# Kernel optimization log

Hardware: AMD Instinct MI355X
Metric: run time of the kernel (lower is better)

The kernel has to match this reference:

```python
import jax, jax.numpy as jnp
import numpy as np
from math import sqrt

DIM = 2048
N_HEADS = 2
HEAD_DIM = DIM // N_HEADS  # 1024 == RoPE dims (dim // 2)
ROPE_DIMS = DIM // 2
ROPE_BASE = 10000.0


def apply_rope(x, dims=ROPE_DIMS, base=ROPE_BASE, offset=0):
    # x: [B, H, L, Dh]; non-traditional (split-half) RoPE over sequence axis
    L = x.shape[-2]
    pos = jnp.arange(offset, offset + L, dtype=x.dtype)[:, None]          # [L,1]
    inv = jnp.exp(jnp.arange(0, dims, 2, dtype=x.dtype) * (-np.log(base) / dims))  # [dims//2]
    theta = pos * inv                                                      # [L, dims//2]
    cos, sin = jnp.cos(theta), jnp.sin(theta)
    h = dims // 2
    x1, x2 = x[..., :h], x[..., h:dims]
    rx1 = x1 * cos - x2 * sin
    rx2 = x1 * sin + x2 * cos
    if dims < x.shape[-1]:
        return jnp.concatenate([rx1, rx2, x[..., dims:]], axis=-1)
    return jnp.concatenate([rx1, rx2], axis=-1)


def setup_inputs() -> dict:
    key = jax.random.key(0)
    ks = jax.random.split(key, 6)
    B, L = 4, 2048
    x = jax.random.normal(ks[0], (B, L, DIM), dtype=jnp.float32)
    # causal additive mask
    causal = jnp.tril(jnp.ones((L, L), dtype=bool))
    mask = jnp.where(causal, 0.0, -1e9).astype(jnp.float32)
    s1 = 1.0 / sqrt(DIM)
    Wqkv_w = jax.random.normal(ks[1], (3 * DIM, DIM), dtype=jnp.float32) * s1
    Wqkv_b = jnp.zeros((3 * DIM,), dtype=jnp.float32)
    out_w = jax.random.normal(ks[2], (DIM, DIM), dtype=jnp.float32) * s1
    out_b = jnp.zeros((DIM,), dtype=jnp.float32)
    return {"x": x, "mask": mask, "Wqkv_w": Wqkv_w, "Wqkv_b": Wqkv_b,
            "out_w": out_w, "out_b": out_b}


def reference(x, mask, Wqkv_w, Wqkv_b, out_w, out_b):
    B, L, D = x.shape
    H, Dh = N_HEADS, HEAD_DIM
    qkv = x @ Wqkv_w.T + Wqkv_b                       # [B, L, 3D]
    q, k, v = jnp.split(qkv, 3, axis=-1)
    # b l (h d) -> b h l d
    split = lambda t: t.reshape(B, L, H, Dh).transpose(0, 2, 1, 3)
    q, k, v = split(q), split(k), split(v)
    q = apply_rope(q)
    k = apply_rope(k)
    scale = sqrt(1.0 / Dh)
    scores = jnp.einsum('bhld,bhkd->bhlk', q * scale, k)  # [B,H,L,L]
    scores = scores + mask                                 # additive causal mask
    probs = jax.nn.softmax(scores, axis=-1)
    vh = jnp.einsum('bhlk,bhkd->bhld', probs, v)
    vh = vh.transpose(0, 2, 1, 3).reshape(B, L, D)         # b h l d -> b l (h d)
    out = vh @ out_w.T + out_b
    return (out, k, v)
```

## Files before the change

kernel.cpp:

```cpp
#include <hip/hip_runtime.h>
#include <hip/hip_bf16.h>
#include <math.h>

typedef unsigned short u16;
typedef __attribute__((ext_vector_type(8))) __bf16 bf16x8;
typedef __attribute__((ext_vector_type(4))) float f32x4;

__device__ __forceinline__ u16 f2b(float f) {
  unsigned u = __builtin_bit_cast(unsigned, f);
  u += 0x7fffu + ((u >> 16) & 1u);
  return (u16)(u >> 16);
}
__device__ __forceinline__ float b2f(u16 h) {
  unsigned u = ((unsigned)h) << 16;
  return __builtin_bit_cast(float, u);
}

__device__ __forceinline__ void gld_lds16(const u16* g, u16* l) {
  __builtin_amdgcn_global_load_lds(
      (const __attribute__((address_space(1))) unsigned int*)g,
      (__attribute__((address_space(3))) unsigned int*)l, 16, 0, 0);
}

template <class FC>
__device__ __forceinline__ void gemm128_body(const u16* A, int lda,
                                             const u16* B, int ldb, FC fc,
                                             int m0, int n0, int K) {
  __shared__ __align__(16) u16 As[128 * 64];
  __shared__ __align__(16) u16 Bs[128 * 64];
  const int tid = threadIdx.x;
  const int wave = tid >> 6;
  const int lane = tid & 63;
  const int srow = lane >> 3;
  const int scol = ((lane & 7) ^ srow) * 8;
  const int wm = (wave & 1) * 64;
  const int wn = (wave >> 1) * 64;
  const int fm = lane & 15;
  const int fs = fm & 7;

  const u16* Abase = A + (size_t)m0 * lda;
  const u16* Bbase = B + (size_t)n0 * ldb;
  const size_t aLane = (size_t)(wave * 8 + srow) * lda + scol;
  const size_t bLane = (size_t)(wave * 8 + srow) * ldb + scol;

  f32x4 acc[4][4];
#pragma unroll
  for (int i = 0; i < 4; ++i)
#pragma unroll
    for (int j = 0; j < 4; ++j) acc[i][j] = (f32x4){0.f, 0.f, 0.f, 0.f};

  for (int k0 = 0; k0 < K; k0 += 64) {
#pragma unroll
    for (int c = 0; c < 4; ++c) {
      gld_lds16(Abase + (aLane + (size_t)(c * 32) * lda + k0),
                &As[(c * 4 + wave) * 512]);
      gld_lds16(Bbase + (bLane + (size_t)(c * 32) * ldb + k0),
                &Bs[(c * 4 + wave) * 512]);
    }
    __syncthreads();
#pragma unroll
    for (int kk = 0; kk < 2; ++kk) {
      const int cb = kk * 4 + (lane >> 4);
      const int p8 = (cb ^ fs) * 8;
      bf16x8 af[4], bfr[4];
#pragma unroll
      for (int i = 0; i < 4; ++i)
        af[i] = *(const bf16x8*)&As[(wm + i * 16 + fm) * 64 + p8];
#pragma unroll
      for (int j = 0; j < 4; ++j)
        bfr[j] = *(const bf16x8*)&Bs[(wn + j * 16 + fm) * 64 + p8];
#pragma unroll
      for (int i = 0; i < 4; ++i)
#pragma unroll
        for (int j = 0; j < 4; ++j)
          acc[i][j] = __builtin_amdgcn_mfma_f32_16x16x32_bf16(
              af[i], bfr[j], acc[i][j], 0, 0, 0);
    }
    __syncthreads();
  }
  const int er = lane >> 4;
#pragma unroll
  for (int i = 0; i < 4; ++i)
#pragma unroll
    for (int j = 0; j < 4; ++j)
#pragma unroll
      for (int r = 0; r < 4; ++r) {
        int m = m0 + wm + i * 16 + er * 4 + r;
        int n = n0 + wn + j * 16 + fm;
        fc(m, n, acc[i][j][r]);
      }
}

struct EQKV {
  u16* qb;
  u16* kb;
  float* vout;
  const float* bias;
  __device__ __forceinline__ void operator()(int m, int n, float v) const {
    v += bias[n];
    int b = m >> 11, l = m & 2047;
    int part = n >> 11, nn = n & 2047, h = nn >> 10, d = nn & 1023;
    size_t idx = ((size_t)((b << 1) + h) * 2048 + l) * 1024 + d;
    if (part == 0)
      qb[idx] = f2b(v);
    else if (part == 1)
      kb[idx] = f2b(v);
    else
      vout[idx] = v;
  }
};
struct EScore {
  float* S;
  __device__ __forceinline__ void operator()(int m, int n, float v) const {
    S[((size_t)m << 11) + n] = v * 0.03125f + (n > m ? -1.0e9f : 0.0f);
  }
};
struct EBf16 {
  u16* o;
  int ld;
  __device__ __forceinline__ void operator()(int m, int n, float v) const {
    o[(size_t)m * ld + n] = f2b(v);
  }
};
struct EOut {
  float* o;
  const float* bias;
  __device__ __forceinline__ void operator()(int m, int n, float v) const {
    o[((size_t)m << 11) + n] = v + bias[n];
  }
};

__global__ void __launch_bounds__(256) k_cast3(const float* x, const float* w1,
                                               const float* w2, u16* xb,
                                               u16* w1b, u16* w2b) {
  long i = (long)(blockIdx.x * 256 + threadIdx.x) * 4;
  const float* src;
  u16* dst;
  long off;
  if (i < 16777216L) {
    src = x; dst = xb; off = i;
  } else if (i < 16777216L + 12582912L) {
    src = w1; dst = w1b; off = i - 16777216L;
  } else {
    src = w2; dst = w2b; off = i - 16777216L - 12582912L;
  }
  float4 f = *(const float4*)(src + off);
  ushort4 o;
  o.x = f2b(f.x);
  o.y = f2b(f.y);
  o.z = f2b(f.z);
  o.w = f2b(f.w);
  *(ushort4*)(dst + off) = o;
}

__global__ void __launch_bounds__(256) k_qkv(const u16* xb, const u16* wb,
                                             const float* bias, u16* qb,
                                             u16* kb, float* vout) {
  gemm128_body(xb, 2048, wb, 2048, EQKV{qb, kb, vout, bias}, blockIdx.y * 128,
               blockIdx.x * 128, 2048);
}

__global__ void __launch_bounds__(256) k_rope(u16* qb, u16* kb, float* kout) {
  int l = blockIdx.x;
  int t = threadIdx.x;
  float lf = (float)l;
  const float c0 = (float)(-9.210340371976184 / 1024.0);
  float s0, c_0, s1, c_1;
  {
    float inv = __expf((float)(2 * t) * c0);
    __sincosf(lf * inv, &s0, &c_0);
    float inv2 = __expf((float)(2 * (t + 256)) * c0);
    __sincosf(lf * inv2, &s1, &c_1);
  }
#pragma unroll
  for (int bh = 0; bh < 8; ++bh) {
    size_t base = ((size_t)bh * 2048 + l) * 1024;
#pragma unroll
    for (int half = 0; half < 2; ++half) {
      int i = t + half * 256;
      float c = half ? c_1 : c_0;
      float s = half ? s1 : s0;
      float x1 = b2f(qb[base + i]), x2 = b2f(qb[base + 512 + i]);
      qb[base + i] = f2b(x1 * c - x2 * s);
      qb[base + 512 + i] = f2b(x1 * s + x2 * c);
      float y1 = b2f(kb[base + i]), y2 = b2f(kb[base + 512 + i]);
      float r1 = y1 * c - y2 * s, r2 = y1 * s + y2 * c;
      kb[base + i] = f2b(r1);
      kb[base + 512 + i] = f2b(r2);
      kout[base + i] = r1;
      kout[base + 512 + i] = r2;
    }
  }
}

__global__ void __launch_bounds__(256) k_transpose_v(const float* v, u16* vt) {
  __shared__ u16 tile[64][65];
  int bh = blockIdx.z;
  int d0 = blockIdx.x * 64, l0 = blockIdx.y * 64;
  const float* vb = v + (size_t)bh * 2048 * 1024;
  u16* vtb = vt + (size_t)bh * 1024 * 2048;
  int t = threadIdx.x;
  int c = t & 63, r4 = t >> 6;
#pragma unroll
  for (int r = 0; r < 16; ++r) {
    int row = r * 4 + r4;
    tile[row][c] = f2b(vb[(size_t)(l0 + row) * 1024 + d0 + c]);
  }
  __syncthreads();
#pragma unroll
  for (int r = 0; r < 16; ++r) {
    int drow = r * 4 + r4;
    vtb[(size_t)(d0 + drow) * 2048 + l0 + c] = tile[c][drow];
  }
}

__global__ void __launch_bounds__(256) k_score(const u16* qb, const u16* kb,
                                               float* S, int zbase) {
  int m0 = blockIdx.y * 128, n0 = blockIdx.x * 128;
  if (n0 > m0) return;
  int z = blockIdx.z, bh = zbase + z;
  const u16* q = qb + (size_t)bh * 2048 * 1024;
  const u16* k = kb + (size_t)bh * 2048 * 1024;
  float* Sz = S + (size_t)z * 2048 * 2048;
  gemm128_body(q, 1024, k, 1024, EScore{Sz}, m0, n0, 1024);
}

__global__ void __launch_bounds__(256) k_softmax(const float* S, u16* P) {
  int l = blockIdx.x, z = blockIdx.y;
  const float* Srow = S + ((size_t)z * 2048 + l) * 2048;
  u16* Prow = P + ((size_t)z * 2048 + l) * 2048;
  int t = threadIdx.x;
  int jend = ((l >> 7) + 1) << 7;
  __shared__ float red[4];
  float vals[8];
  float mx = -1e30f;
#pragma unroll
  for (int i = 0; i < 8; ++i) {
    int j = i * 256 + t;
    float v = (j <= l) ? Srow[j] : -1e30f;
    vals[i] = v;
    mx = fmaxf(mx, v);
  }
#pragma unroll
  for (int off = 32; off; off >>= 1) mx = fmaxf(mx, __shfl_down(mx, off));
  if ((t & 63) == 0) red[t >> 6] = mx;
  __syncthreads();
  mx = fmaxf(fmaxf(red[0], red[1]), fmaxf(red[2], red[3]));
  __syncthreads();
  float sum = 0.f;
#pragma unroll
  for (int i = 0; i < 8; ++i) {
    int j = i * 256 + t;
    float e = (j <= l) ? __expf(vals[i] - mx) : 0.f;
    vals[i] = e;
    sum += e;
  }
#pragma unroll
  for (int off = 32; off; off >>= 1) sum += __shfl_down(sum, off);
  if ((t & 63) == 0) red[t >> 6] = sum;
  __syncthreads();
  sum = red[0] + red[1] + red[2] + red[3];
  float is = 1.0f / sum;
#pragma unroll
  for (int i = 0; i < 8; ++i) {
    int j = i * 256 + t;
    if (j < jend) Prow[j] = f2b(vals[i] * is);
  }
}

__global__ void __launch_bounds__(256) k_pv(const u16* P, const u16* vt,
                                            u16* vh, int zbase) {
  int z = blockIdx.z, bh = zbase + z;
  int b = bh >> 1, h = bh & 1;
  int m0 = blockIdx.y * 128, n0 = blockIdx.x * 128;
  const u16* Pz = P + (size_t)z * 2048 * 2048;
  const u16* vtb = vt + (size_t)bh * 1024 * 2048;
  u16* outb = vh + (size_t)b * 2048 * 2048 + (size_t)h * 1024;
  int Keff = m0 + 128;
  gemm128_body(Pz, 2048, vtb, 2048, EBf16{outb, 2048}, m0, n0, Keff);
}

__global__ void __launch_bounds__(256) k_out(const u16* vh, const u16* w2,
                                             const float* bias, float* out) {
  gemm128_body(vh, 2048, w2, 2048, EOut{out, bias}, blockIdx.y * 128,
               blockIdx.x * 128, 2048);
}

extern "C" void kernel_launch(void* const* d_in, const int* in_sizes, int n_in,
                              void* d_out, int out_size, void* d_ws,
                              size_t ws_size, hipStream_t stream) {
  const float* x = (const float*)d_in[0];
  const float* w1 = (const float*)d_in[2];
  const float* b1 = (const float*)d_in[3];
  const float* w2 = (const float*)d_in[4];
  const float* b2 = (const float*)d_in[5];
  float* out = (float*)d_out;
  float* kout = out + (size_t)16777216;
  float* vout = kout + (size_t)16777216;

  char* ws = (char*)d_ws;
  u16* xb = (u16*)ws;
  ws += (size_t)33554432;
  u16* w1b = (u16*)ws;
  ws += (size_t)25165824;
  u16* w2b = (u16*)ws;
  ws += (size_t)8388608;
  u16* qb = (u16*)ws;
  ws += (size_t)33554432;
  u16* kb = (u16*)ws;
  ws += (size_t)33554432;
  u16* vtb = (u16*)ws;
  ws += (size_t)33554432;
  u16* vh = (u16*)ws;
  ws += (size_t)33554432;
  size_t used = (size_t)(ws - (char*)d_ws);
  size_t rem = ws_size > used ? ws_size - used : 0;
  size_t perz = (size_t)2048 * 2048 * 4 + (size_t)2048 * 2048 * 2;
  int Z = 1;
  if (rem >= 8 * perz)
    Z = 8;
  else if (rem >= 4 * perz)
    Z = 4;
  else if (rem >= 2 * perz)
    Z = 2;
  float* S = (float*)ws;
  u16* P = (u16*)(ws + (size_t)Z * 2048 * 2048 * 4);

  k_cast3<<<32768, 256, 0, stream>>>(x, w1, w2, xb, w1b, w2b);
  k_qkv<<<dim3(48, 64), 256, 0, stream>>>(xb, w1b, b1, qb, kb, vout);
  k_rope<<<2048, 256, 0, stream>>>(qb, kb, kout);
  k_transpose_v<<<dim3(16, 32, 8), 256, 0, stream>>>(vout, vtb);
  for (int zb = 0; zb < 8; zb += Z) {
    k_score<<<dim3(16, 16, Z), 256, 0, stream>>>(qb, kb, S, zb);
    k_softmax<<<dim3(2048, Z), 256, 0, stream>>>(S, P);
    k_pv<<<dim3(8, 16, Z), 256, 0, stream>>>(P, vtb, vh, zb);
  }
  k_out<<<dim3(16, 64), 256, 0, stream>>>(vh, w2b, b2, out);
}
```

Measured before the change: 877.6 us.

## Store attention scores in bf16 in place and batch all heads per launch

The score GEMM now writes masked, scaled scores as bf16 instead of fp32. Softmax then overwrites them in place with bf16 probabilities, so the separate fp32 S and bf16 P buffers are gone. Workspace is reused by aliasing the score buffers onto the dead xb and a freed region, and vh onto qb. This allows all 8 batch-heads to run in a single launch of each of score, softmax and PV instead of a workspace-dependent loop. The aim is to halve score memory traffic and cut launch count. The cost is rounding pre-softmax logits to bf16, which adds numerical error.

```diff
diff --git a/kernel.cpp b/kernel.cpp
--- a/kernel.cpp
+++ b/kernel.cpp
@@ -109,10 +109,10 @@
       vout[idx] = v;
   }
 };
-struct EScore {
-  float* S;
+struct EScoreB {
+  u16* S;
   __device__ __forceinline__ void operator()(int m, int n, float v) const {
-    S[((size_t)m << 11) + n] = v * 0.03125f + (n > m ? -1.0e9f : 0.0f);
+    S[((size_t)m << 11) + n] = f2b(v * 0.03125f + (n > m ? -1.0e9f : 0.0f));
   }
 };
 struct EBf16 {
@@ -129,6 +129,10 @@
     o[((size_t)m << 11) + n] = v + bias[n];
   }
 };
+
+__device__ __forceinline__ u16* spz(u16* sp0, u16* sp1, int z) {
+  return (z < 4) ? sp0 + (size_t)z * 4194304 : sp1 + (size_t)(z - 4) * 4194304;
+}
 
 __global__ void __launch_bounds__(256) k_cast3(const float* x, const float* w1,
                                                const float* w2, u16* xb,
@@ -215,20 +219,18 @@
 }
 
 __global__ void __launch_bounds__(256) k_score(const u16* qb, const u16* kb,
-                                               float* S, int zbase) {
+                                               u16* sp0, u16* sp1) {
   int m0 = blockIdx.y * 128, n0 = blockIdx.x * 128;
   if (n0 > m0) return;
-  int z = blockIdx.z, bh = zbase + z;
-  const u16* q = qb + (size_t)bh * 2048 * 1024;
-  const u16* k = kb + (size_t)bh * 2048 * 1024;
-  float* Sz = S + (size_t)z * 2048 * 2048;
-  gemm128_body(q, 1024, k, 1024, EScore{Sz}, m0, n0, 1024);
-}
-
-__global__ void __launch_bounds__(256) k_softmax(const float* S, u16* P) {
+  int z = blockIdx.z;
+  const u16* q = qb + (size_t)z * 2048 * 1024;
+  const u16* k = kb + (size_t)z * 2048 * 1024;
+  gemm128_body(q, 1024, k, 1024, EScoreB{spz(sp0, sp1, z)}, m0, n0, 1024);
+}
+
+__global__ void __launch_bounds__(256) k_softmax(u16* sp0, u16* sp1) {
   int l = blockIdx.x, z = blockIdx.y;
-  const float* Srow = S + ((size_t)z * 2048 + l) * 2048;
-  u16* Prow = P + ((size_t)z * 2048 + l) * 2048;
+  u16* row = spz(sp0, sp1, z) + ((size_t)l << 11);
   int t = threadIdx.x;
   int jend = ((l >> 7) + 1) << 7;
   __shared__ float red[4];
@@ -237,7 +239,7 @@
 #pragma unroll
   for (int i = 0; i < 8; ++i) {
     int j = i * 256 + t;
-    float v = (j <= l) ? Srow[j] : -1e30f;
+    float v = (j <= l) ? b2f(row[j]) : -1e30f;
     vals[i] = v;
     mx = fmaxf(mx, v);
   }
@@ -264,17 +266,17 @@
 #pragma unroll
   for (int i = 0; i < 8; ++i) {
     int j = i * 256 + t;
-    if (j < jend) Prow[j] = f2b(vals[i] * is);
-  }
-}
-
-__global__ void __launch_bounds__(256) k_pv(const u16* P, const u16* vt,
-                                            u16* vh, int zbase) {
-  int z = blockIdx.z, bh = zbase + z;
-  int b = bh >> 1, h = bh & 1;
+    if (j < jend) row[j] = f2b(vals[i] * is);
+  }
+}
+
+__global__ void __launch_bounds__(256) k_pv(u16* sp0, u16* sp1, const u16* vt,
+                                            u16* vh) {
+  int z = blockIdx.z;
+  int b = z >> 1, h = z & 1;
   int m0 = blockIdx.y * 128, n0 = blockIdx.x * 128;
-  const u16* Pz = P + (size_t)z * 2048 * 2048;
-  const u16* vtb = vt + (size_t)bh * 1024 * 2048;
+  const u16* Pz = spz(sp0, sp1, z);
+  const u16* vtb = vt + (size_t)z * 1024 * 2048;
   u16* outb = vh + (size_t)b * 2048 * 2048 + (size_t)h * 1024;
   int Keff = m0 + 128;
   gemm128_body(Pz, 2048, vtb, 2048, EBf16{outb, 2048}, m0, n0, Keff);
@@ -311,29 +313,16 @@
   ws += (size_t)33554432;
   u16* vtb = (u16*)ws;
   ws += (size_t)33554432;
-  u16* vh = (u16*)ws;
-  ws += (size_t)33554432;
-  size_t used = (size_t)(ws - (char*)d_ws);
-  size_t rem = ws_size > used ? ws_size - used : 0;
-  size_t perz = (size_t)2048 * 2048 * 4 + (size_t)2048 * 2048 * 2;
-  int Z = 1;
-  if (rem >= 8 * perz)
-    Z = 8;
-  else if (rem >= 4 * perz)
-    Z = 4;
-  else if (rem >= 2 * perz)
-    Z = 2;
-  float* S = (float*)ws;
-  u16* P = (u16*)(ws + (size_t)Z * 2048 * 2048 * 4);
+  u16* sp1 = (u16*)ws;
+  u16* sp0 = xb;
+  u16* vh = qb;
 
   k_cast3<<<32768, 256, 0, stream>>>(x, w1, w2, xb, w1b, w2b);
   k_qkv<<<dim3(48, 64), 256, 0, stream>>>(xb, w1b, b1, qb, kb, vout);
   k_rope<<<2048, 256, 0, stream>>>(qb, kb, kout);
   k_transpose_v<<<dim3(16, 32, 8), 256, 0, stream>>>(vout, vtb);
-  for (int zb = 0; zb < 8; zb += Z) {
-    k_score<<<dim3(16, 16, Z), 256, 0, stream>>>(qb, kb, S, zb);
-    k_softmax<<<dim3(2048, Z), 256, 0, stream>>>(S, P);
-    k_pv<<<dim3(8, 16, Z), 256, 0, stream>>>(P, vtb, vh, zb);
-  }
+  k_score<<<dim3(16, 16, 8), 256, 0, stream>>>(qb, kb, sp0, sp1);
+  k_softmax<<<dim3(2048, 8), 256, 0, stream>>>(sp0, sp1);
+  k_pv<<<dim3(8, 16, 8), 256, 0, stream>>>(sp0, sp1, vtb, vh);
   k_out<<<dim3(16, 64), 256, 0, stream>>>(vh, w2b, b2, out);
 }
```

Result: no change. 860.8 us (-1.9%).
